# Optimization experiments

Measured on AMD Instinct MI355X. Metric: run time of the kernel, lower is better.

The kernel has to match this reference:

```python
import jax, jax.numpy as jnp
import numpy as np

B, S, D_IN, D_OUT = 4, 2048, 4096, 4096
E = 32        # n_loras (number of LoRA experts)
R = 16        # per-expert rank; E*R == rmoe == 512
K = 2         # top_k
SCALING = 32.0 / 16.0  # lora_alpha / r (use_rslora=False)


def setup_inputs() -> dict:
    key = jax.random.key(0)
    ks = jax.random.split(key, 5)
    x = jax.random.normal(ks[0], (B, S, D_IN), dtype=jnp.float32)
    base_w = jax.random.normal(ks[1], (D_OUT, D_IN), dtype=jnp.float32) * 0.02
    gate_w = jax.random.normal(ks[2], (E, D_IN), dtype=jnp.float32) * 0.02
    lora_A = jax.random.normal(ks[3], (E * R, D_IN), dtype=jnp.float32) * 0.02
    lora_B = jax.random.normal(ks[4], (D_OUT, E * R), dtype=jnp.float32) * 0.02
    return {"x": x, "base_w": base_w, "gate_w": gate_w, "lora_A": lora_A, "lora_B": lora_B}


def reference(x, base_w, gate_w, lora_A, lora_B):
    # Base linear layer (nn.Linear, no bias)
    base = jnp.einsum('bsd,od->bso', x, base_w)

    # Gating: softmax over n_loras experts, top-k selection, renormalize
    logits = jnp.einsum('bsd,ed->bse', x, gate_w)              # [B,S,E]
    probs = jax.nn.softmax(logits, axis=-1)
    vals, idx = jax.lax.top_k(probs, K)                         # [B,S,K]
    vals = vals / jnp.sum(vals, axis=-1, keepdims=True)
    # Dense per-expert weight (zero for unselected experts)
    w = jnp.sum(jax.nn.one_hot(idx, E, dtype=x.dtype) * vals[..., None], axis=-2)  # [B,S,E]

    # Shared stacked LoRA: lora_A rows / lora_B cols are per-expert rank-R blocks
    ax = jnp.einsum('bsd,rd->bsr', x, lora_A).reshape(B, S, E, R)   # [B,S,E,R]
    b_blk = lora_B.T.reshape(E, R, D_OUT)                           # [E,R,out]
    delta = jnp.einsum('bser,ero->bso', ax * w[..., None], b_blk) * SCALING

    return base + delta
```

## Files before the change

kernel.cpp:

```cpp
#include <hip/hip_runtime.h>


#define D_IN   4096
#define D_OUT  4096
#define NTOK   8192
#define NE     32
#define RMOE   512
#define KCAT   4608
#define SCALING 2.0f

typedef unsigned short u16;
typedef __attribute__((ext_vector_type(4))) float  f32x4;
typedef __attribute__((ext_vector_type(4))) unsigned short u16x4;
typedef __attribute__((ext_vector_type(8))) short  bf16x8;

__device__ __forceinline__ u16 f2bf(float f) {
  unsigned u = __float_as_uint(f);
  u += 0x7FFFu + ((u >> 16) & 1u);
  return (u16)(u >> 16);
}

__device__ __forceinline__ void gload16(const void* g, void* l) {
  __builtin_amdgcn_global_load_lds(
      (const __attribute__((address_space(1))) unsigned*)g,
      (__attribute__((address_space(3))) unsigned*)l, 16, 0, 0);
}

#define BAR() do { asm volatile("" ::: "memory"); \
                   __builtin_amdgcn_s_barrier();  \
                   asm volatile("" ::: "memory"); } while (0)
#define WAITV8() asm volatile("s_waitcnt vmcnt(8)" ::: "memory")
#define WAITV4() asm volatile("s_waitcnt vmcnt(4)" ::: "memory")
#define WAITV0() asm volatile("s_waitcnt vmcnt(0)" ::: "memory")

#define TT 32
#define KC 256

__global__ __launch_bounds__(256) void k_logits(
    const float* __restrict__ x, const float* __restrict__ gate_w,
    float* __restrict__ wdense, u16* __restrict__ xb)
{
  __shared__ float smem[2 * TT * KC];
  __shared__ float lgt[TT * 36];
  __shared__ int   e1s[TT]; __shared__ int   e2s[TT];
  __shared__ float w1s[TT]; __shared__ float w2s[TT];
  float* xs = smem;
  float* gs = smem + TT * KC;

  const int tid  = threadIdx.x;
  const int lane = tid & 63, wave = tid >> 6;
  const int ks = lane >> 4, tg = (lane >> 2) & 3, eg = lane & 3;
  const int row0 = blockIdx.x * TT;
  const int kc0 = wave * 16 + ks * 4;

  float acc[8][8];
#pragma unroll
  for (int t = 0; t < 8; ++t)
#pragma unroll
    for (int e = 0; e < 8; ++e) acc[t][e] = 0.f;

  for (int kt = 0; kt < D_IN / KC; ++kt) {
    __syncthreads();
#pragma unroll
    for (int i = 0; i < 8; ++i) {
      int c = tid + i * 256;
      int tok = c >> 6, kq = c & 63;
      f32x4 v = ((const f32x4*)(x + (size_t)(row0 + tok) * D_IN + kt * KC))[kq];
      *(f32x4*)&xs[tok * KC + ((kq ^ (tok >> 3)) << 2)] = v;
      u16x4 h;
      h[0] = f2bf(v[0]); h[1] = f2bf(v[1]); h[2] = f2bf(v[2]); h[3] = f2bf(v[3]);
      ((u16x4*)(xb + (size_t)(row0 + tok) * KCAT + kt * KC))[kq] = h;
    }
#pragma unroll
    for (int i = 0; i < 8; ++i) {
      int c = tid + i * 256;
      int e = c >> 6, kq = c & 63;
      f32x4 v = ((const f32x4*)(gate_w + (size_t)e * D_IN + kt * KC))[kq];
      *(f32x4*)&gs[e * KC + ((kq ^ (e >> 3)) << 2)] = v;
    }
    __syncthreads();
#pragma unroll
    for (int j = 0; j < 4; ++j) {
      const int Kc = kc0 + j;
      f32x4 xv[8], gv[8];
#pragma unroll
      for (int t = 0; t < 8; ++t)
        xv[t] = *(const f32x4*)&xs[(tg * 8 + t) * KC + ((Kc ^ tg) << 2)];
#pragma unroll
      for (int e = 0; e < 8; ++e)
        gv[e] = *(const f32x4*)&gs[(eg * 8 + e) * KC + ((Kc ^ eg) << 2)];
#pragma unroll
      for (int t = 0; t < 8; ++t)
#pragma unroll
        for (int e = 0; e < 8; ++e)
#pragma unroll
          for (int m = 0; m < 4; ++m)
            acc[t][e] += xv[t][m] * gv[e][m];
    }
  }

#pragma unroll
  for (int t = 0; t < 8; ++t)
#pragma unroll
    for (int e = 0; e < 8; ++e) {
      float v = acc[t][e];
      v += __shfl_xor(v, 16);
      v += __shfl_xor(v, 32);
      acc[t][e] = v;
    }
  __syncthreads();
  float* red = smem;
  if (ks == 0) {
#pragma unroll
    for (int t = 0; t < 8; ++t)
#pragma unroll
      for (int e4 = 0; e4 < 8; e4 += 4) {
        f32x4 v = { acc[t][e4], acc[t][e4 + 1], acc[t][e4 + 2], acc[t][e4 + 3] };
        *(f32x4*)&red[(wave * 16 + tg * 4 + eg) * 64 + t * 8 + e4] = v;
      }
  }
  __syncthreads();
  {
    int tok = tid >> 3, e4 = (tid & 7) << 2;
    f32x4 s = {0.f, 0.f, 0.f, 0.f};
#pragma unroll
    for (int w = 0; w < 4; ++w)
      s += *(const f32x4*)&red[(w * 16 + (tok >> 3) * 4 + (e4 >> 3)) * 64 + (tok & 7) * 8 + (e4 & 7)];
    *(f32x4*)&lgt[tok * 36 + e4] = s;
  }
  __syncthreads();
  if (tid < TT) {
    float l1 = -1e30f; int e1 = 0;
    for (int e = 0; e < NE; ++e) { float v = lgt[tid * 36 + e]; if (v > l1) { l1 = v; e1 = e; } }
    float l2 = -1e30f; int e2 = 0;
    for (int e = 0; e < NE; ++e) { if (e == e1) continue; float v = lgt[tid * 36 + e]; if (v > l2) { l2 = v; e2 = e; } }
    float t = __expf(l2 - l1);
    float w2 = t / (1.f + t);
    e1s[tid] = e1; e2s[tid] = e2; w1s[tid] = 1.f - w2; w2s[tid] = w2;
  }
  __syncthreads();
#pragma unroll
  for (int i = 0; i < 4; ++i) {
    int c = tid + i * 256;
    int tok = c >> 5, e = c & 31;
    float v = (e == e1s[tok]) ? w1s[tok] : (e == e2s[tok]) ? w2s[tok] : 0.f;
    wdense[(size_t)(row0 + tok) * NE + e] = v;
  }
}

__global__ __launch_bounds__(256) void k_wconv(
    const float* __restrict__ base_w, const float* __restrict__ lora_B,
    const float* __restrict__ lora_A, u16* __restrict__ wb, u16* __restrict__ la)
{
  const int bid = blockIdx.x, tid = threadIdx.x;
  if (bid < D_OUT) {
    const float* src = base_w + (size_t)bid * D_IN;
    u16* dst = wb + (size_t)bid * KCAT;
#pragma unroll
    for (int i = 0; i < 4; ++i) {
      int c = tid + i * 256;
      f32x4 v = ((const f32x4*)src)[c];
      u16x4 h; h[0] = f2bf(v[0]); h[1] = f2bf(v[1]); h[2] = f2bf(v[2]); h[3] = f2bf(v[3]);
      ((u16x4*)dst)[c] = h;
    }
    if (tid < 128) {
      f32x4 v = ((const f32x4*)(lora_B + (size_t)bid * RMOE))[tid];
      u16x4 h; h[0] = f2bf(v[0]); h[1] = f2bf(v[1]); h[2] = f2bf(v[2]); h[3] = f2bf(v[3]);
      ((u16x4*)(dst + D_IN))[tid] = h;
    }
  } else {
    int r = bid - D_OUT;
    const float* src = lora_A + (size_t)r * D_IN;
    u16* dst = la + (size_t)r * D_IN;
#pragma unroll
    for (int i = 0; i < 4; ++i) {
      int c = tid + i * 256;
      f32x4 v = ((const f32x4*)src)[c];
      u16x4 h; h[0] = f2bf(v[0]); h[1] = f2bf(v[1]); h[2] = f2bf(v[2]); h[3] = f2bf(v[3]);
      ((u16x4*)dst)[c] = h;
    }
  }
}

__global__ __launch_bounds__(256) void k_gemm_ax(
    const u16* __restrict__ A, const u16* __restrict__ Bw,
    const float* __restrict__ wdense, u16* __restrict__ xb)
{
  __shared__ u16 sh[49152];
  const int nbx = RMOE / 128;
  const int nwg = gridDim.x;
  int bid = blockIdx.x;
  int wg = (bid & 7) * (nwg >> 3) + (bid >> 3);
  const int tm = wg / nbx, tn = wg % nbx;
  const int tid = threadIdx.x;
  const int lane = tid & 63, wave = tid >> 6;
  const int wr = wave >> 1, wc = wave & 1;
  const int l15 = lane & 15, g = lane >> 4;
  const int row0 = tm * 128, col0 = tn * 128;

  size_t offA[4], offB[4]; int dstd[4];
#pragma unroll
  for (int i = 0; i < 4; ++i) {
    int c = tid + i * 256;
    int r = c >> 3, s = (c & 7) ^ (r & 7);
    offA[i] = (size_t)(row0 + r) * KCAT + s * 8;
    offB[i] = (size_t)(col0 + r) * D_IN + s * 8;
    dstd[i] = c * 8;
  }

#define STGAX(b, kt) do { \
    _Pragma("unroll") for (int i = 0; i < 4; ++i) { \
      gload16(A  + offA[i] + (size_t)(kt) * 64, &sh[(b) * 16384 + dstd[i]]); \
      gload16(Bw + offB[i] + (size_t)(kt) * 64, &sh[(b) * 16384 + 8192 + dstd[i]]); } } while (0)

  f32x4 acc[4][4];
#pragma unroll
  for (int i = 0; i < 4; ++i)
#pragma unroll
    for (int j = 0; j < 4; ++j) acc[i][j] = (f32x4){0.f, 0.f, 0.f, 0.f};

  STGAX(0, 0);
  STGAX(1, 1);
  WAITV8();
  BAR();

  const int swz = (g ^ (l15 & 7)) * 8;
  for (int kt = 0; kt < D_IN / 64; ++kt) {
    if (kt + 2 < D_IN / 64) STGAX((kt + 2) % 3, kt + 2);
    const u16* As_ = &sh[(kt % 3) * 16384];
    const u16* Bs_ = &sh[(kt % 3) * 16384 + 8192];
    bf16x8 af[4][2], bfr[4][2];
#pragma unroll
    for (int i = 0; i < 4; ++i) {
      int ixa = (wr * 64 + i * 16 + l15) * 64 + swz;
      af[i][0] = *(const bf16x8*)&As_[ixa]; af[i][1] = *(const bf16x8*)&As_[ixa ^ 32];
      int ixb = (wc * 64 + i * 16 + l15) * 64 + swz;
      bfr[i][0] = *(const bf16x8*)&Bs_[ixb]; bfr[i][1] = *(const bf16x8*)&Bs_[ixb ^ 32];
    }
    __builtin_amdgcn_s_setprio(1);
#pragma unroll
    for (int i = 0; i < 4; ++i)
#pragma unroll
      for (int j = 0; j < 4; ++j)
#pragma unroll
        for (int kk = 0; kk < 2; ++kk)
          acc[i][j] = __builtin_amdgcn_mfma_f32_16x16x32_bf16(af[i][kk], bfr[j][kk], acc[i][j], 0, 0, 0);
    __builtin_amdgcn_s_setprio(0);
    if (kt >= D_IN / 64 - 2) WAITV0(); else WAITV8();
    BAR();
  }
#undef STGAX

#pragma unroll
  for (int i = 0; i < 4; ++i) {
    int rbase = row0 + wr * 64 + i * 16 + (g << 2);
#pragma unroll
    for (int j = 0; j < 4; ++j) {
      int cb = col0 + wc * 64 + j * 16 + l15;
#pragma unroll
      for (int q = 0; q < 4; ++q) {
        int trow = rbase + q;
        float wgt = wdense[(size_t)trow * NE + (cb >> 4)];
        xb[(size_t)trow * KCAT + D_IN + cb] = f2bf(acc[i][j][q] * wgt * SCALING);
      }
    }
  }
}

#define NT (KCAT / 64)

__global__ __launch_bounds__(512, 2) void k_gemm_main(
    const u16* __restrict__ A, const u16* __restrict__ Bw, float* __restrict__ C)
{
  __shared__ u16 sh[65536];

  const int tid  = threadIdx.x;
  const int lane = tid & 63;
  const int wv   = tid >> 6;
  const int wm   = wv >> 2;
  const int wn   = wv & 3;
  const int l15  = lane & 15, g = lane >> 4;

  const int nwg = gridDim.x;
  int bid = blockIdx.x;
  int wg = (bid & 7) * (nwg >> 3) + (bid >> 3);
  const int tn = wg & 15, tm = wg >> 4;

  const int rsw   = (g ^ (l15 & 7)) * 8;
  const int aBase = l15 * 64 + rsw;
  const int bBase = ((wn & 1) * 64 + l15) * 64 + rsw;

  const int c0 = tid, c1 = tid + 512;
  const int r0s = c0 >> 3, s0s = (c0 & 7) ^ (r0s & 7);
  const int r1s = c1 >> 3, s1s = (c1 & 7) ^ (r1s & 7);
  const size_t offc0 = (size_t)r0s * KCAT + s0s * 8;
  const size_t offc1 = (size_t)r1s * KCAT + s1s * 8;
  const u16* pA0a = A  + (size_t)(tm * 256 +   0) * KCAT + offc0;
  const u16* pA0b = A  + (size_t)(tm * 256 +   0) * KCAT + offc1;
  const u16* pA1a = A  + (size_t)(tm * 256 + 128) * KCAT + offc0;
  const u16* pA1b = A  + (size_t)(tm * 256 + 128) * KCAT + offc1;
  const u16* pB0a = Bw + (size_t)(tn * 256 +   0) * KCAT + offc0;
  const u16* pB0b = Bw + (size_t)(tn * 256 +   0) * KCAT + offc1;
  const u16* pB1a = Bw + (size_t)(tn * 256 + 128) * KCAT + offc0;
  const u16* pB1b = Bw + (size_t)(tn * 256 + 128) * KCAT + offc1;
  const int d0 = c0 * 8, d1 = c1 * 8;

#define STG(pa, pb, base) do { \
    gload16((pa), &sh[(base) + d0]); \
    gload16((pb), &sh[(base) + d1]); \
    (pa) += 64; (pb) += 64; } while (0)

#define MM4x2(MO, NO, AF, BF) do { \
    _Pragma("unroll") for (int m_ = 0; m_ < 4; ++m_) \
    _Pragma("unroll") for (int n_ = 0; n_ < 2; ++n_) \
    _Pragma("unroll") for (int kk_ = 0; kk_ < 2; ++kk_) \
      acc[m_ + (MO)][n_ + (NO)] = __builtin_amdgcn_mfma_f32_16x16x32_bf16( \
          AF[m_][kk_], BF[n_][kk_], acc[m_ + (MO)][n_ + (NO)], 0, 0, 0); } while (0)

  f32x4 acc[8][4];
#pragma unroll
  for (int i = 0; i < 8; ++i)
#pragma unroll
    for (int j = 0; j < 4; ++j) acc[i][j] = (f32x4){0.f, 0.f, 0.f, 0.f};

  STG(pA0a, pA0b,     0);
  STG(pB0a, pB0b, 16384);
  STG(pA1a, pA1b,  8192);
  STG(pB1a, pB1b, 24576);
  STG(pA0a, pA0b, 32768 +     0);
  STG(pB0a, pB0b, 32768 + 16384);
  WAITV4();
  BAR();

  bf16x8 aA[4][2], aB[4][2], bR[2][2];
  {
    const int shA = (wm << 13);
    const int shB = 16384 + ((wn >> 1) << 13);
#pragma unroll
    for (int m = 0; m < 4; ++m) {
      int ix = shA + aBase + m * 1024;
      aA[m][0] = *(const bf16x8*)&sh[ix]; aA[m][1] = *(const bf16x8*)&sh[ix ^ 32];
    }
#pragma unroll
    for (int n = 0; n < 2; ++n) {
      int ix = shB + bBase + n * 1024;
      bR[n][0] = *(const bf16x8*)&sh[ix]; bR[n][1] = *(const bf16x8*)&sh[ix ^ 32];
    }
  }

  for (int u = 0; u < NT; ++u) {
    const int cb = (u & 1) << 15;
    const int nb = cb ^ 32768;
    const int shA  = cb + (wm << 13);
    const int shB  = cb + 16384 + ((wn >> 1) << 13);
    const int shAn = nb + (wm << 13);
    const int shBn = nb + 16384 + ((wn >> 1) << 13);

    if (u < NT - 1) STG(pA1a, pA1b, nb + 8192);
#pragma unroll
    for (int m = 0; m < 4; ++m) {
      int ix = shA + aBase + (m + 4) * 1024;
      aB[m][0] = *(const bf16x8*)&sh[ix]; aB[m][1] = *(const bf16x8*)&sh[ix ^ 32];
    }
    BAR();
    __builtin_amdgcn_s_setprio(1);
    MM4x2(0, 0, aA, bR);
    __builtin_amdgcn_s_setprio(0);
    BAR();

    if (u < NT - 1) STG(pB1a, pB1b, nb + 24576);
    BAR();
    __builtin_amdgcn_s_setprio(1);
    MM4x2(4, 0, aB, bR);
    __builtin_amdgcn_s_setprio(0);
#pragma unroll
    for (int n = 0; n < 2; ++n) {
      int ix = shB + bBase + (n + 2) * 1024;
      bR[n][0] = *(const bf16x8*)&sh[ix]; bR[n][1] = *(const bf16x8*)&sh[ix ^ 32];
    }
    BAR();

    if (u < NT - 2) STG(pA0a, pA0b, cb + 0);
    BAR();
    __builtin_amdgcn_s_setprio(1);
    MM4x2(4, 2, aB, bR);
    __builtin_amdgcn_s_setprio(0);
    BAR();

    if (u < NT - 2) { STG(pB0a, pB0b, cb + 16384); WAITV4(); }
    else            { WAITV0(); }
    BAR();
    __builtin_amdgcn_s_setprio(1);
    MM4x2(0, 2, aA, bR);
    __builtin_amdgcn_s_setprio(0);
    if (u < NT - 1) {
#pragma unroll
      for (int m = 0; m < 4; ++m) {
        int ix = shAn + aBase + m * 1024;
        aA[m][0] = *(const bf16x8*)&sh[ix]; aA[m][1] = *(const bf16x8*)&sh[ix ^ 32];
      }
#pragma unroll
      for (int n = 0; n < 2; ++n) {
        int ix = shBn + bBase + n * 1024;
        bR[n][0] = *(const bf16x8*)&sh[ix]; bR[n][1] = *(const bf16x8*)&sh[ix ^ 32];
      }
    }
    BAR();
  }
#undef STG
#undef MM4x2

  const int crow0 = tm * 256 + wm * 128 + g * 4;
  const int ccol0 = tn * 256 + wn * 64 + l15;
#pragma unroll
  for (int mf = 0; mf < 8; ++mf)
#pragma unroll
    for (int n = 0; n < 4; ++n)
#pragma unroll
      for (int q = 0; q < 4; ++q)
        C[(size_t)(crow0 + mf * 16 + q) * D_OUT + ccol0 + n * 16] = acc[mf][n][q];
}

extern "C" void kernel_launch(void* const* d_in, const int* in_sizes, int n_in,
                              void* d_out, int out_size, void* d_ws, size_t ws_size,
                              hipStream_t stream) {
  const float* x      = (const float*)d_in[0];
  const float* base_w = (const float*)d_in[1];
  const float* gate_w = (const float*)d_in[2];
  const float* lora_A = (const float*)d_in[3];
  const float* lora_B = (const float*)d_in[4];
  float* out = (float*)d_out;

  char* ws = (char*)d_ws;
  u16* xb       = (u16*)ws;
  u16* wb       = (u16*)(ws + 75497472);
  u16* la       = (u16*)(ws + 75497472 + 37748736);
  float* wdense = (float*)(ws + 75497472 + 37748736 + 4194304);

  hipLaunchKernelGGL(k_logits,    dim3(NTOK / TT),    dim3(256), 0, stream, x, gate_w, wdense, xb);
  hipLaunchKernelGGL(k_wconv,     dim3(D_OUT + RMOE), dim3(256), 0, stream, base_w, lora_B, lora_A, wb, la);
  hipLaunchKernelGGL(k_gemm_ax,   dim3((NTOK/128) * (RMOE/128)),  dim3(256), 0, stream, xb, la, wdense, xb);
  hipLaunchKernelGGL(k_gemm_main, dim3((NTOK/256) * (D_OUT/256)), dim3(512), 0, stream, xb, wb, out);
}
```

Measured before the change: 384.3 us.

## Use 32x32 MFMA in main GEMM, merge prep kernels, shrink ax tiles

Result: slower. 429.4 us (+11.8%).

```diff
diff --git a/kernel.cpp b/kernel.cpp
--- a/kernel.cpp
+++ b/kernel.cpp
@@ -10,9 +10,10 @@
 #define SCALING 2.0f
 
 typedef unsigned short u16;
-typedef __attribute__((ext_vector_type(4))) float  f32x4;
-typedef __attribute__((ext_vector_type(4))) unsigned short u16x4;
-typedef __attribute__((ext_vector_type(8))) short  bf16x8;
+typedef __attribute__((ext_vector_type(4)))  float  f32x4;
+typedef __attribute__((ext_vector_type(16))) float  f32x16;
+typedef __attribute__((ext_vector_type(4)))  unsigned short u16x4;
+typedef __attribute__((ext_vector_type(8)))  short  bf16x8;
 
 __device__ __forceinline__ u16 f2bf(float f) {
   unsigned u = __float_as_uint(f);
@@ -29,25 +30,60 @@
 #define BAR() do { asm volatile("" ::: "memory"); \
                    __builtin_amdgcn_s_barrier();  \
                    asm volatile("" ::: "memory"); } while (0)
-#define WAITV8() asm volatile("s_waitcnt vmcnt(8)" ::: "memory")
+#define WAITV6() asm volatile("s_waitcnt vmcnt(6)" ::: "memory")
 #define WAITV4() asm volatile("s_waitcnt vmcnt(4)" ::: "memory")
 #define WAITV0() asm volatile("s_waitcnt vmcnt(0)" ::: "memory")
 
 #define TT 32
 #define KC 256
 
-__global__ __launch_bounds__(256) void k_logits(
+__global__ __launch_bounds__(256) void k_prep(
     const float* __restrict__ x, const float* __restrict__ gate_w,
-    float* __restrict__ wdense, u16* __restrict__ xb)
+    const float* __restrict__ base_w, const float* __restrict__ lora_B,
+    const float* __restrict__ lora_A,
+    float* __restrict__ wdense, u16* __restrict__ xb,
+    u16* __restrict__ wb, u16* __restrict__ la)
 {
   __shared__ float smem[2 * TT * KC];
   __shared__ float lgt[TT * 36];
   __shared__ int   e1s[TT]; __shared__ int   e2s[TT];
   __shared__ float w1s[TT]; __shared__ float w2s[TT];
+  const int tid = threadIdx.x;
+
+  if (blockIdx.x >= 256) {
+    const int bid = blockIdx.x - 256;
+    if (bid < D_OUT) {
+      const float* src = base_w + (size_t)bid * D_IN;
+      u16* dst = wb + (size_t)bid * KCAT;
+#pragma unroll
+      for (int i = 0; i < 4; ++i) {
+        int c = tid + i * 256;
+        f32x4 v = ((const f32x4*)src)[c];
+        u16x4 h; h[0] = f2bf(v[0]); h[1] = f2bf(v[1]); h[2] = f2bf(v[2]); h[3] = f2bf(v[3]);
+        ((u16x4*)dst)[c] = h;
+      }
+      if (tid < 128) {
+        f32x4 v = ((const f32x4*)(lora_B + (size_t)bid * RMOE))[tid];
+        u16x4 h; h[0] = f2bf(v[0]); h[1] = f2bf(v[1]); h[2] = f2bf(v[2]); h[3] = f2bf(v[3]);
+        ((u16x4*)(dst + D_IN))[tid] = h;
+      }
+    } else {
+      int r = bid - D_OUT;
+      const float* src = lora_A + (size_t)r * D_IN;
+      u16* dst = la + (size_t)r * D_IN;
+#pragma unroll
+      for (int i = 0; i < 4; ++i) {
+        int c = tid + i * 256;
+        f32x4 v = ((const f32x4*)src)[c];
+        u16x4 h; h[0] = f2bf(v[0]); h[1] = f2bf(v[1]); h[2] = f2bf(v[2]); h[3] = f2bf(v[3]);
+        ((u16x4*)dst)[c] = h;
+      }
+    }
+    return;
+  }
+
   float* xs = smem;
   float* gs = smem + TT * KC;
-
-  const int tid  = threadIdx.x;
   const int lane = tid & 63, wave = tid >> 6;
   const int ks = lane >> 4, tg = (lane >> 2) & 3, eg = lane & 3;
   const int row0 = blockIdx.x * TT;
@@ -148,115 +184,89 @@
   }
 }
 
-__global__ __launch_bounds__(256) void k_wconv(
-    const float* __restrict__ base_w, const float* __restrict__ lora_B,
-    const float* __restrict__ lora_A, u16* __restrict__ wb, u16* __restrict__ la)
-{
-  const int bid = blockIdx.x, tid = threadIdx.x;
-  if (bid < D_OUT) {
-    const float* src = base_w + (size_t)bid * D_IN;
-    u16* dst = wb + (size_t)bid * KCAT;
-#pragma unroll
-    for (int i = 0; i < 4; ++i) {
-      int c = tid + i * 256;
-      f32x4 v = ((const f32x4*)src)[c];
-      u16x4 h; h[0] = f2bf(v[0]); h[1] = f2bf(v[1]); h[2] = f2bf(v[2]); h[3] = f2bf(v[3]);
-      ((u16x4*)dst)[c] = h;
-    }
-    if (tid < 128) {
-      f32x4 v = ((const f32x4*)(lora_B + (size_t)bid * RMOE))[tid];
-      u16x4 h; h[0] = f2bf(v[0]); h[1] = f2bf(v[1]); h[2] = f2bf(v[2]); h[3] = f2bf(v[3]);
-      ((u16x4*)(dst + D_IN))[tid] = h;
-    }
-  } else {
-    int r = bid - D_OUT;
-    const float* src = lora_A + (size_t)r * D_IN;
-    u16* dst = la + (size_t)r * D_IN;
-#pragma unroll
-    for (int i = 0; i < 4; ++i) {
-      int c = tid + i * 256;
-      f32x4 v = ((const f32x4*)src)[c];
-      u16x4 h; h[0] = f2bf(v[0]); h[1] = f2bf(v[1]); h[2] = f2bf(v[2]); h[3] = f2bf(v[3]);
-      ((u16x4*)dst)[c] = h;
-    }
-  }
-}
-
 __global__ __launch_bounds__(256) void k_gemm_ax(
-    const u16* __restrict__ A, const u16* __restrict__ Bw,
+    const u16* __restrict__ A, const u16* __restrict__ La,
     const float* __restrict__ wdense, u16* __restrict__ xb)
 {
-  __shared__ u16 sh[49152];
-  const int nbx = RMOE / 128;
+  __shared__ u16 sh[36864];
   const int nwg = gridDim.x;
   int bid = blockIdx.x;
   int wg = (bid & 7) * (nwg >> 3) + (bid >> 3);
-  const int tm = wg / nbx, tn = wg % nbx;
+  const int tm = wg >> 2, tn = wg & 3;
   const int tid = threadIdx.x;
-  const int lane = tid & 63, wave = tid >> 6;
-  const int wr = wave >> 1, wc = wave & 1;
+  const int lane = tid & 63, wn = tid >> 6;
   const int l15 = lane & 15, g = lane >> 4;
-  const int row0 = tm * 128, col0 = tn * 128;
-
-  size_t offA[4], offB[4]; int dstd[4];
+  const int row0 = tm * 64, col0 = tn * 128;
+
+  size_t offA[2], offB[4]; int dA[2], dB[4];
+#pragma unroll
+  for (int i = 0; i < 2; ++i) {
+    int c = tid + i * 256;
+    int r = c >> 3, s = (c & 7) ^ (r & 7);
+    offA[i] = (size_t)(row0 + r) * KCAT + s * 8;
+    dA[i] = c * 8;
+  }
 #pragma unroll
   for (int i = 0; i < 4; ++i) {
     int c = tid + i * 256;
     int r = c >> 3, s = (c & 7) ^ (r & 7);
-    offA[i] = (size_t)(row0 + r) * KCAT + s * 8;
     offB[i] = (size_t)(col0 + r) * D_IN + s * 8;
-    dstd[i] = c * 8;
+    dB[i] = c * 8;
   }
 
 #define STGAX(b, kt) do { \
-    _Pragma("unroll") for (int i = 0; i < 4; ++i) { \
-      gload16(A  + offA[i] + (size_t)(kt) * 64, &sh[(b) * 16384 + dstd[i]]); \
-      gload16(Bw + offB[i] + (size_t)(kt) * 64, &sh[(b) * 16384 + 8192 + dstd[i]]); } } while (0)
-
-  f32x4 acc[4][4];
+    _Pragma("unroll") for (int i = 0; i < 2; ++i) \
+      gload16(A  + offA[i] + (size_t)(kt) * 64, &sh[(b) * 12288 + dA[i]]); \
+    _Pragma("unroll") for (int i = 0; i < 4; ++i) \
+      gload16(La + offB[i] + (size_t)(kt) * 64, &sh[(b) * 12288 + 4096 + dB[i]]); } while (0)
+
+  f32x4 acc[4][2];
 #pragma unroll
   for (int i = 0; i < 4; ++i)
 #pragma unroll
-    for (int j = 0; j < 4; ++j) acc[i][j] = (f32x4){0.f, 0.f, 0.f, 0.f};
+    for (int j = 0; j < 2; ++j) acc[i][j] = (f32x4){0.f, 0.f, 0.f, 0.f};
 
   STGAX(0, 0);
   STGAX(1, 1);
-  WAITV8();
+  WAITV6();
   BAR();
 
   const int swz = (g ^ (l15 & 7)) * 8;
   for (int kt = 0; kt < D_IN / 64; ++kt) {
     if (kt + 2 < D_IN / 64) STGAX((kt + 2) % 3, kt + 2);
-    const u16* As_ = &sh[(kt % 3) * 16384];
-    const u16* Bs_ = &sh[(kt % 3) * 16384 + 8192];
-    bf16x8 af[4][2], bfr[4][2];
+    const u16* As_ = &sh[(kt % 3) * 12288];
+    const u16* Bs_ = &sh[(kt % 3) * 12288 + 4096];
+    bf16x8 af[4][2], bfr[2][2];
 #pragma unroll
     for (int i = 0; i < 4; ++i) {
-      int ixa = (wr * 64 + i * 16 + l15) * 64 + swz;
+      int ixa = (i * 16 + l15) * 64 + swz;
       af[i][0] = *(const bf16x8*)&As_[ixa]; af[i][1] = *(const bf16x8*)&As_[ixa ^ 32];
-      int ixb = (wc * 64 + i * 16 + l15) * 64 + swz;
-      bfr[i][0] = *(const bf16x8*)&Bs_[ixb]; bfr[i][1] = *(const bf16x8*)&Bs_[ixb ^ 32];
+    }
+#pragma unroll
+    for (int j = 0; j < 2; ++j) {
+      int ixb = (wn * 32 + j * 16 + l15) * 64 + swz;
+      bfr[j][0] = *(const bf16x8*)&Bs_[ixb]; bfr[j][1] = *(const bf16x8*)&Bs_[ixb ^ 32];
     }
     __builtin_amdgcn_s_setprio(1);
 #pragma unroll
     for (int i = 0; i < 4; ++i)
 #pragma unroll
-      for (int j = 0; j < 4; ++j)
+      for (int j = 0; j < 2; ++j)
 #pragma unroll
         for (int kk = 0; kk < 2; ++kk)
           acc[i][j] = __builtin_amdgcn_mfma_f32_16x16x32_bf16(af[i][kk], bfr[j][kk], acc[i][j], 0, 0, 0);
     __builtin_amdgcn_s_setprio(0);
-    if (kt >= D_IN / 64 - 2) WAITV0(); else WAITV8();
+    if (kt >= D_IN / 64 - 2) WAITV0(); else WAITV6();
     BAR();
   }
 #undef STGAX
 
 #pragma unroll
   for (int i = 0; i < 4; ++i) {
-    int rbase = row0 + wr * 64 + i * 16 + (g << 2);
-#pragma unroll
-    for (int j = 0; j < 4; ++j) {
-      int cb = col0 + wc * 64 + j * 16 + l15;
+    int rbase = row0 + i * 16 + (g << 2);
+#pragma unroll
+    for (int j = 0; j < 2; ++j) {
+      int cb = col0 + wn * 32 + j * 16 + l15;
 #pragma unroll
       for (int q = 0; q < 4; ++q) {
         int trow = rbase + q;
@@ -279,16 +289,16 @@
   const int wv   = tid >> 6;
   const int wm   = wv >> 2;
   const int wn   = wv & 3;
-  const int l15  = lane & 15, g = lane >> 4;
+  const int r32  = lane & 31, g2 = lane >> 5;
 
   const int nwg = gridDim.x;
   int bid = blockIdx.x;
   int wg = (bid & 7) * (nwg >> 3) + (bid >> 3);
   const int tn = wg & 15, tm = wg >> 4;
 
-  const int rsw   = (g ^ (l15 & 7)) * 8;
-  const int aBase = l15 * 64 + rsw;
-  const int bBase = ((wn & 1) * 64 + l15) * 64 + rsw;
+  const int slot0 = (g2 ^ (r32 & 7)) * 8;
+  const int aBase = r32 * 64 + slot0;
+  const int bBase = ((wn & 1) * 64 + r32) * 64 + slot0;
 
   const int c0 = tid, c1 = tid + 512;
   const int r0s = c0 >> 3, s0s = (c0 & 7) ^ (r0s & 7);
@@ -310,18 +320,30 @@
     gload16((pb), &sh[(base) + d1]); \
     (pa) += 64; (pb) += 64; } while (0)
 
-#define MM4x2(MO, NO, AF, BF) do { \
-    _Pragma("unroll") for (int m_ = 0; m_ < 4; ++m_) \
-    _Pragma("unroll") for (int n_ = 0; n_ < 2; ++n_) \
-    _Pragma("unroll") for (int kk_ = 0; kk_ < 2; ++kk_) \
-      acc[m_ + (MO)][n_ + (NO)] = __builtin_amdgcn_mfma_f32_16x16x32_bf16( \
-          AF[m_][kk_], BF[n_][kk_], acc[m_ + (MO)][n_ + (NO)], 0, 0, 0); } while (0)
-
-  f32x4 acc[8][4];
-#pragma unroll
-  for (int i = 0; i < 8; ++i)
-#pragma unroll
-    for (int j = 0; j < 4; ++j) acc[i][j] = (f32x4){0.f, 0.f, 0.f, 0.f};
+#define MM2x4(MO, NO, AF) do { \
+    _Pragma("unroll") for (int ks_ = 0; ks_ < 4; ++ks_) \
+    _Pragma("unroll") for (int m_ = 0; m_ < 2; ++m_) \
+      acc[m_ + (MO)][NO] = __builtin_amdgcn_mfma_f32_32x32x16_bf16( \
+          AF[m_][ks_], bR[ks_], acc[m_ + (MO)][NO], 0, 0, 0); } while (0)
+
+#define RDA(DST, MI0, SH) do { \
+    _Pragma("unroll") for (int m_ = 0; m_ < 2; ++m_) { \
+      int ix_ = (SH) + aBase + ((MI0) + m_) * 2048; \
+      _Pragma("unroll") for (int ks_ = 0; ks_ < 4; ++ks_) \
+        DST[m_][ks_] = *(const bf16x8*)&sh[ix_ ^ (ks_ * 16)]; } } while (0)
+
+#define RDB(NI, SH) do { \
+      int ix_ = (SH) + bBase + (NI) * 2048; \
+      _Pragma("unroll") for (int ks_ = 0; ks_ < 4; ++ks_) \
+        bR[ks_] = *(const bf16x8*)&sh[ix_ ^ (ks_ * 16)]; } while (0)
+
+  f32x16 acc[4][2];
+#pragma unroll
+  for (int i = 0; i < 4; ++i)
+#pragma unroll
+    for (int j = 0; j < 2; ++j)
+      acc[i][j] = (f32x16){0.f,0.f,0.f,0.f, 0.f,0.f,0.f,0.f,
+                           0.f,0.f,0.f,0.f, 0.f,0.f,0.f,0.f};
 
   STG(pA0a, pA0b,     0);
   STG(pB0a, pB0b, 16384);
@@ -332,21 +354,9 @@
   WAITV4();
   BAR();
 
-  bf16x8 aA[4][2], aB[4][2], bR[2][2];
-  {
-    const int shA = (wm << 13);
-    const int shB = 16384 + ((wn >> 1) << 13);
-#pragma unroll
-    for (int m = 0; m < 4; ++m) {
-      int ix = shA + aBase + m * 1024;
-      aA[m][0] = *(const bf16x8*)&sh[ix]; aA[m][1] = *(const bf16x8*)&sh[ix ^ 32];
-    }
-#pragma unroll
-    for (int n = 0; n < 2; ++n) {
-      int ix = shB + bBase + n * 1024;
-      bR[n][0] = *(const bf16x8*)&sh[ix]; bR[n][1] = *(const bf16x8*)&sh[ix ^ 32];
-    }
-  }
+  bf16x8 aLo[2][4], aHi[2][4], bR[4];
+  RDA(aLo, 0, (wm << 13));
+  RDB(0, 16384 + ((wn >> 1) << 13));
 
   for (int u = 0; u < NT; ++u) {
     const int cb = (u & 1) << 15;
@@ -357,33 +367,25 @@
     const int shBn = nb + 16384 + ((wn >> 1) << 13);
 
     if (u < NT - 1) STG(pA1a, pA1b, nb + 8192);
-#pragma unroll
-    for (int m = 0; m < 4; ++m) {
-      int ix = shA + aBase + (m + 4) * 1024;
-      aB[m][0] = *(const bf16x8*)&sh[ix]; aB[m][1] = *(const bf16x8*)&sh[ix ^ 32];
-    }
+    RDA(aHi, 2, shA);
     BAR();
     __builtin_amdgcn_s_setprio(1);
-    MM4x2(0, 0, aA, bR);
+    MM2x4(0, 0, aLo);
     __builtin_amdgcn_s_setprio(0);
     BAR();
 
     if (u < NT - 1) STG(pB1a, pB1b, nb + 24576);
     BAR();
     __builtin_amdgcn_s_setprio(1);
-    MM4x2(4, 0, aB, bR);
+    MM2x4(2, 0, aHi);
     __builtin_amdgcn_s_setprio(0);
-#pragma unroll
-    for (int n = 0; n < 2; ++n) {
-      int ix = shB + bBase + (n + 2) * 1024;
-      bR[n][0] = *(const bf16x8*)&sh[ix]; bR[n][1] = *(const bf16x8*)&sh[ix ^ 32];
-    }
+    RDB(1, shB);
     BAR();
 
     if (u < NT - 2) STG(pA0a, pA0b, cb + 0);
     BAR();
     __builtin_amdgcn_s_setprio(1);
-    MM4x2(4, 2, aB, bR);
+    MM2x4(2, 1, aHi);
     __builtin_amdgcn_s_setprio(0);
     BAR();
 
@@ -391,34 +393,29 @@
     else            { WAITV0(); }
     BAR();
     __builtin_amdgcn_s_setprio(1);
-    MM4x2(0, 2, aA, bR);
+    MM2x4(0, 1, aLo);
     __builtin_amdgcn_s_setprio(0);
     if (u < NT - 1) {
-#pragma unroll
-      for (int m = 0; m < 4; ++m) {
-        int ix = shAn + aBase + m * 1024;
-        aA[m][0] = *(const bf16x8*)&sh[ix]; aA[m][1] = *(const bf16x8*)&sh[ix ^ 32];
-      }
-#pragma unroll
-      for (int n = 0; n < 2; ++n) {
-        int ix = shBn + bBase + n * 1024;
-        bR[n][0] = *(const bf16x8*)&sh[ix]; bR[n][1] = *(const bf16x8*)&sh[ix ^ 32];
-      }
+      RDA(aLo, 0, shAn);
+      RDB(0, shBn);
     }
     BAR();
   }
 #undef STG
-#undef MM4x2
-
-  const int crow0 = tm * 256 + wm * 128 + g * 4;
-  const int ccol0 = tn * 256 + wn * 64 + l15;
-#pragma unroll
-  for (int mf = 0; mf < 8; ++mf)
-#pragma unroll
-    for (int n = 0; n < 4; ++n)
-#pragma unroll
-      for (int q = 0; q < 4; ++q)
-        C[(size_t)(crow0 + mf * 16 + q) * D_OUT + ccol0 + n * 16] = acc[mf][n][q];
+#undef MM2x4
+#undef RDA
+#undef RDB
+
+  const int crow0 = tm * 256 + wm * 128 + 4 * g2;
+  const int ccol0 = tn * 256 + wn * 64 + r32;
+#pragma unroll
+  for (int mi = 0; mi < 4; ++mi)
+#pragma unroll
+    for (int ni = 0; ni < 2; ++ni)
+#pragma unroll
+      for (int r = 0; r < 16; ++r)
+        C[(size_t)(crow0 + mi * 32 + (r & 3) + 8 * (r >> 2)) * D_OUT
+          + ccol0 + ni * 32] = acc[mi][ni][r];
 }
 
 extern "C" void kernel_launch(void* const* d_in, const int* in_sizes, int n_in,
@@ -437,8 +434,10 @@
   u16* la       = (u16*)(ws + 75497472 + 37748736);
   float* wdense = (float*)(ws + 75497472 + 37748736 + 4194304);
 
-  hipLaunchKernelGGL(k_logits,    dim3(NTOK / TT),    dim3(256), 0, stream, x, gate_w, wdense, xb);
-  hipLaunchKernelGGL(k_wconv,     dim3(D_OUT + RMOE), dim3(256), 0, stream, base_w, lora_B, lora_A, wb, la);
-  hipLaunchKernelGGL(k_gemm_ax,   dim3((NTOK/128) * (RMOE/128)),  dim3(256), 0, stream, xb, la, wdense, xb);
-  hipLaunchKernelGGL(k_gemm_main, dim3((NTOK/256) * (D_OUT/256)), dim3(512), 0, stream, xb, wb, out);
-}
+  hipLaunchKernelGGL(k_prep,      dim3(256 + D_OUT + RMOE), dim3(256), 0, stream,
+                     x, gate_w, base_w, lora_B, lora_A, wdense, xb, wb, la);
+  hipLaunchKernelGGL(k_gemm_ax,   dim3((NTOK/64) * (RMOE/128)),  dim3(256), 0, stream,
+                     xb, la, wdense, xb);
+  hipLaunchKernelGGL(k_gemm_main, dim3((NTOK/256) * (D_OUT/256)), dim3(512), 0, stream,
+                     xb, wb, out);
+}
```
